# Kernel tuning notes

Hardware: AMD Instinct MI355X
Metric: run time of the kernel (lower is better)

## Reference

```python
import jax, jax.numpy as jnp
import numpy as np
from jax import lax

U = 64          # LSTM units (hard-coded in Actor)
EPS = 1e-12     # tf.contrib layer_norm default epsilon


def _ln(x, g, b):
    # layer norm over last axis; g,b broadcast
    mu = jnp.mean(x, axis=-1, keepdims=True)
    var = jnp.mean(jnp.square(x - mu), axis=-1, keepdims=True)
    return (x - mu) * jax.lax.rsqrt(var + EPS) * g + b


def _lstm_layer(xs, W, gamma, beta, gc, bc):
    # xs: (B, T, D); W: (D+U, 4U); gamma,beta: (4, U); gc,bc: (U,)
    B = xs.shape[0]
    c0 = jnp.zeros((B, U), xs.dtype)
    h0 = jnp.zeros((B, U), xs.dtype)

    def step(carry, x_t):
        c, h = carry
        z = jnp.concatenate([x_t, h], axis=-1) @ W          # (B, 4U), no bias
        z = _ln(z.reshape(B, 4, U), gamma, beta)            # per-gate layer norm
        i, j, f, o = z[:, 0], z[:, 1], z[:, 2], z[:, 3]
        new_c = c * jax.nn.sigmoid(f + 1.0) + jax.nn.sigmoid(i) * jnp.tanh(j)
        new_h = jnp.tanh(_ln(new_c, gc, bc)) * jax.nn.sigmoid(o)
        return (new_c, new_h), new_h

    _, hs = lax.scan(step, (c0, h0), jnp.swapaxes(xs, 0, 1))  # hs: (T, B, U)
    return jnp.swapaxes(hs, 0, 1)                             # (B, T, U)


def setup_inputs() -> dict:
    key = jax.random.key(0)
    ks = jax.random.split(key, 8)
    B, T, D, A = 256, 1024, 128, 16
    s1 = 1.0 / np.sqrt(D + U)
    s2 = 1.0 / np.sqrt(U + U)
    return {
        "obss": jax.random.normal(ks[0], (B, T, D), jnp.float32),
        "W1": jax.random.uniform(ks[1], (D + U, 4 * U), jnp.float32, -s1, s1),
        "gamma1": jnp.ones((4, U), jnp.float32),
        "beta1": jnp.zeros((4, U), jnp.float32),
        "gc1": jnp.ones((U,), jnp.float32),
        "bc1": jnp.zeros((U,), jnp.float32),
        "W2": jax.random.uniform(ks[2], (U + U, 4 * U), jnp.float32, -s2, s2),
        "gamma2": jnp.ones((4, U), jnp.float32),
        "beta2": jnp.zeros((4, U), jnp.float32),
        "gc2": jnp.ones((U,), jnp.float32),
        "bc2": jnp.zeros((U,), jnp.float32),
        "Wd": jax.random.uniform(ks[3], (U, A), jnp.float32, -0.003, 0.003),
        "bd": jnp.zeros((A,), jnp.float32),
    }


def reference(obss, W1, gamma1, beta1, gc1, bc1, W2, gamma2, beta2, gc2, bc2, Wd, bd):
    h1 = _lstm_layer(obss, W1, gamma1, beta1, gc1, bc1)   # (B, T, U)
    h2 = _lstm_layer(h1, W2, gamma2, beta2, gc2, bc2)     # (B, T, U)
    return jnp.tanh(h2 @ Wd + bd)                          # (B, T, nb_actions)
```

## Files before the change

### kernel.cpp

```cpp
#include <hip/hip_runtime.h>
#include <math.h>

#define TT 1024
#define DD 128
#define UU 64

__device__ __forceinline__ float sigm(float x) {
    return __builtin_amdgcn_rcpf(1.0f + __expf(-x));
}
__device__ __forceinline__ float tanhfast(float x) {
    float e = __expf(2.0f * x);
    return fmaf(-2.0f, __builtin_amdgcn_rcpf(e + 1.0f), 1.0f);
}

template<int CTRL>
__device__ __forceinline__ float dpp_add(float v) {
    return v + __int_as_float(__builtin_amdgcn_update_dpp(
        0, __float_as_int(v), CTRL, 0xf, 0xf, true));
}
__device__ __forceinline__ float wave_red_sum(float v) {
    v = dpp_add<0x111>(v);
    v = dpp_add<0x112>(v);
    v = dpp_add<0x114>(v);
    v = dpp_add<0x118>(v);
    v = dpp_add<0x142>(v);
    v = dpp_add<0x143>(v);
    return __int_as_float(__builtin_amdgcn_readlane(__float_as_int(v), 63));
}

#define DOT64(res, vptr, WARR) do {                                \
    const float4* _v4 = (const float4*)(vptr);                     \
    float _a0 = 0.f, _a1 = 0.f, _a2 = 0.f, _a3 = 0.f;              \
    _Pragma("unroll")                                              \
    for (int _k = 0; _k < UU / 4; ++_k) {                          \
        float4 _hv = _v4[_k];                                      \
        _a0 = fmaf(_hv.x, WARR[4 * _k + 0], _a0);                  \
        _a1 = fmaf(_hv.y, WARR[4 * _k + 1], _a1);                  \
        _a2 = fmaf(_hv.z, WARR[4 * _k + 2], _a2);                  \
        _a3 = fmaf(_hv.w, WARR[4 * _k + 3], _a3);                  \
    }                                                              \
    res = (_a0 + _a1) + (_a2 + _a3);                               \
} while (0)

__global__ __launch_bounds__(256, 1)
void xgemm(const float* __restrict__ obss, const float* __restrict__ W1,
           float* __restrict__ z1x, int t0, int chsh)
{
    const int tid = threadIdx.x;
    const int CH = 1 << chsh;
    __shared__ __align__(16) float xs[64 * DD];

    const int rbase = blockIdx.x * 64;
    for (int i = tid; i < 64 * (DD / 4); i += 256) {
        int rr = i >> 5;
        int k4 = i & 31;
        int r  = rbase + rr;
        int b  = r >> chsh;
        int tl = r & (CH - 1);
        ((float4*)xs)[rr * 32 + k4] =
            ((const float4*)(obss + ((size_t)b * TT + t0 + tl) * DD))[k4];
    }

    float w[DD];
    #pragma unroll
    for (int k = 0; k < DD; ++k) w[k] = W1[k * 256 + tid];
    __syncthreads();

    for (int rr = 0; rr < 64; rr += 2) {
        float a0=0,a1=0,a2=0,a3=0, b0=0,b1=0,b2=0,b3=0;
        const float4* x0 = (const float4*)(xs + rr * DD);
        const float4* x1 = (const float4*)(xs + (rr + 1) * DD);
        #pragma unroll
        for (int k4 = 0; k4 < DD / 4; ++k4) {
            float4 xv = x0[k4], yv = x1[k4];
            a0 = fmaf(xv.x, w[4*k4+0], a0);
            a1 = fmaf(xv.y, w[4*k4+1], a1);
            a2 = fmaf(xv.z, w[4*k4+2], a2);
            a3 = fmaf(xv.w, w[4*k4+3], a3);
            b0 = fmaf(yv.x, w[4*k4+0], b0);
            b1 = fmaf(yv.y, w[4*k4+1], b1);
            b2 = fmaf(yv.z, w[4*k4+2], b2);
            b3 = fmaf(yv.w, w[4*k4+3], b3);
        }
        size_t r = (size_t)rbase + rr;
        z1x[r * 256 + tid]       = (a0 + a1) + (a2 + a3);
        z1x[(r + 1) * 256 + tid] = (b0 + b1) + (b2 + b3);
    }
}

__global__ __launch_bounds__(768) __attribute__((amdgpu_waves_per_eu(3, 3)))
void lstm_rec(const float* __restrict__ z1x,
              const float* __restrict__ W1, const float* __restrict__ W2,
              const float* __restrict__ gamma1, const float* __restrict__ beta1,
              const float* __restrict__ gc1, const float* __restrict__ bc1,
              const float* __restrict__ gamma2, const float* __restrict__ beta2,
              const float* __restrict__ gc2, const float* __restrict__ bc2,
              const float* __restrict__ Wd, const float* __restrict__ bd,
              float* __restrict__ out, float* __restrict__ state,
              int t0, int nsteps)
{
    const int tid  = threadIdx.x;
    const int b    = blockIdx.x;
    const int gid  = tid >> 8;
    const int stid = tid & 255;
    const int lane = stid & 63;
    const int wav  = stid >> 6;

    __shared__ __align__(16) float zsA[256], zsB[256], z2xs[256];
    __shared__ __align__(16) float h1ring[2][UU];
    __shared__ __align__(16) float h1p[4][UU], h2p[4][UU];
    __shared__ __align__(16) float h2hist[32 * 65];
    __shared__ __align__(16) float wds[UU * 16];
    __shared__ float bds[16];

    float* st = state + (size_t)b * 256;
    const int NS = nsteps;

    if (gid == 0) {
        float w1h[UU];
        #pragma unroll
        for (int k = 0; k < UU; ++k) w1h[k] = W1[(DD + k) * 256 + stid];
        const float g1 = gamma1[stid], bb1 = beta1[stid];
        const float gcl = gc1[lane],  bcl = bc1[lane];

        float c1, h1v = 0.f;
        if (t0 == 0) { c1 = 0.f; h1p[wav][lane] = 0.f; }
        else         { c1 = st[lane]; h1v = st[64 + lane]; h1p[wav][lane] = h1v; }

        const float* zrow = z1x + (size_t)b * NS * 256;
        float zx = zrow[stid];
        __syncthreads();

        #pragma unroll 1
        for (int n = 0; n <= NS + 2; ++n) {
            float zxn = zx;
            if (n < NS) {
                int tnl = (n + 1 < NS) ? n + 1 : n;
                zxn = zrow[(size_t)tnl * 256 + stid];

                float zdot;
                DOT64(zdot, h1p[wav], w1h);
                float z = zx + zdot;
                float s = wave_red_sum(z);
                float q = wave_red_sum(z * z);
                float mu  = s * (1.f/64.f);
                float var = q * (1.f/64.f) - mu * mu;
                float zn  = (z - mu) * __builtin_amdgcn_rsqf(var + 1e-12f) * g1 + bb1;
                zsA[stid] = (wav == 1) ? tanhfast(zn)
                          : (wav == 2) ? sigm(zn + 1.f)
                          :              sigm(zn);
            }
            __syncthreads();
            if (n < NS) {
                float ai = zsA[lane],       aj = zsA[64 + lane];
                float af = zsA[128 + lane], ao = zsA[192 + lane];
                c1 = c1 * af + ai * aj;
                float cs = wave_red_sum(c1);
                float cq = wave_red_sum(c1 * c1);
                float cmu  = cs * (1.f/64.f);
                float cvar = cq * (1.f/64.f) - cmu * cmu;
                float cn   = (c1 - cmu) * __builtin_amdgcn_rsqf(cvar + 1e-12f) * gcl + bcl;
                h1v = tanhfast(cn) * ao;
                h1p[wav][lane] = h1v;
                if (wav == 0) h1ring[n & 1][lane] = h1v;
            }
            __syncthreads();
            zx = zxn;
        }
        if (t0 + NS < TT && wav == 0) {
            st[lane]      = c1;
            st[64 + lane] = h1v;
        }
    } else if (gid == 1) {
        float w2x[UU];
        #pragma unroll
        for (int k = 0; k < UU; ++k) w2x[k] = W2[k * 256 + stid];
        for (int i = stid; i < UU * 16; i += 256) wds[i] = Wd[i];
        if (stid < 16) bds[stid] = bd[stid];
        __syncthreads();

        #pragma unroll 1
        for (int n = 0; n <= NS + 2; ++n) {
            if (n >= 1 && n <= NS) {
                float zxdot;
                DOT64(zxdot, h1ring[(n - 1) & 1], w2x);
                z2xs[stid] = zxdot;
            }
            __syncthreads();
            if ((n & 15) == 2 && n >= 18) {
                int rloc = stid >> 4;
                int a    = stid & 15;
                int m    = n - 18 + rloc;
                float o = bds[a];
                const float* hrow = &h2hist[(m & 31) * 65];
                #pragma unroll
                for (int k = 0; k < UU; ++k)
                    o = fmaf(hrow[k], wds[k * 16 + a], o);
                out[((size_t)b * TT + (t0 + m)) * 16 + a] = tanhfast(o);
            }
            __syncthreads();
        }
    } else {
        float w2h[UU];
        #pragma unroll
        for (int k = 0; k < UU; ++k) w2h[k] = W2[(UU + k) * 256 + stid];
        const float g2 = gamma2[stid], bb2 = beta2[stid];
        const float gcl = gc2[lane],  bcl = bc2[lane];

        float c2, h2v = 0.f;
        if (t0 == 0) { c2 = 0.f; h2p[wav][lane] = 0.f; }
        else         { c2 = st[128 + lane]; h2v = st[192 + lane]; h2p[wav][lane] = h2v; }
        float z2h = 0.f;
        if (t0 != 0) { DOT64(z2h, h2p[wav], w2h); }
        __syncthreads();

        #pragma unroll 1
        for (int n = 0; n <= NS + 2; ++n) {
            if (n >= 2 && n <= NS + 1) {
                float ai = zsB[lane],       aj = zsB[64 + lane];
                float af = zsB[128 + lane], ao = zsB[192 + lane];
                c2 = c2 * af + ai * aj;
                float cs = wave_red_sum(c2);
                float cq = wave_red_sum(c2 * c2);
                float cmu  = cs * (1.f/64.f);
                float cvar = cq * (1.f/64.f) - cmu * cmu;
                float cn   = (c2 - cmu) * __builtin_amdgcn_rsqf(cvar + 1e-12f) * gcl + bcl;
                h2v = tanhfast(cn) * ao;
                h2p[wav][lane] = h2v;
                if (wav == 0) h2hist[((n - 2) & 31) * 65 + lane] = h2v;
                DOT64(z2h, h2p[wav], w2h);
            }
            __syncthreads();
            if (n >= 1 && n <= NS) {
                float z2 = z2xs[stid] + z2h;
                float s2 = wave_red_sum(z2);
                float q2 = wave_red_sum(z2 * z2);
                float mu2  = s2 * (1.f/64.f);
                float var2 = q2 * (1.f/64.f) - mu2 * mu2;
                float zn2  = (z2 - mu2) * __builtin_amdgcn_rsqf(var2 + 1e-12f) * g2 + bb2;
                zsB[stid] = (wav == 1) ? tanhfast(zn2)
                          : (wav == 2) ? sigm(zn2 + 1.f)
                          :              sigm(zn2);
            }
            __syncthreads();
        }
        if (t0 + NS < TT && wav == 0) {
            st[128 + lane] = c2;
            st[192 + lane] = h2v;
        }
    }
}

extern "C" void kernel_launch(void* const* d_in, const int* in_sizes, int n_in,
                              void* d_out, int out_size, void* d_ws, size_t ws_size,
                              hipStream_t stream) {
    (void)in_sizes; (void)n_in; (void)out_size;
    const float* obss   = (const float*)d_in[0];
    const float* W1     = (const float*)d_in[1];
    const float* gamma1 = (const float*)d_in[2];
    const float* beta1  = (const float*)d_in[3];
    const float* gc1    = (const float*)d_in[4];
    const float* bc1    = (const float*)d_in[5];
    const float* W2     = (const float*)d_in[6];
    const float* gamma2 = (const float*)d_in[7];
    const float* beta2  = (const float*)d_in[8];
    const float* gc2    = (const float*)d_in[9];
    const float* bc2    = (const float*)d_in[10];
    const float* Wd     = (const float*)d_in[11];
    const float* bd     = (const float*)d_in[12];
    float* out = (float*)d_out;

    float* state = (float*)d_ws;
    float* z1x   = (float*)((char*)d_ws + (size_t)256 * 256 * sizeof(float));

    int CH = 16;
    for (int c = TT; c >= 16; c >>= 1) {
        size_t need = (size_t)256 * c * 256 * sizeof(float)
                    + (size_t)256 * 256 * sizeof(float);
        if (need <= ws_size) { CH = c; break; }
    }
    int chsh = 31 - __builtin_clz((unsigned)CH);

    for (int t0 = 0; t0 < TT; t0 += CH) {
        xgemm<<<(256 * CH) / 64, 256, 0, stream>>>(obss, W1, z1x, t0, chsh);
        lstm_rec<<<256, 768, 0, stream>>>(z1x, W1, W2,
                                          gamma1, beta1, gc1, bc1,
                                          gamma2, beta2, gc2, bc2,
                                          Wd, bd, out, state, t0, CH);
    }
}
```

Before: 1.348 ms.

## Broadcast hidden state via readlane and move recurrent weights out of registers

The 64-float per-thread weight arrays are replaced. The recurrent weights for both layers now sit in shared memory as float4 and are read each step, and the layer-2 input weights are read straight from global memory (cached). The hidden state is no longer written to and reloaded from shared memory; each lane's value is broadcast with readlane inside the dot product. This cuts register pressure and an LDS round trip on the serial recurrence path, but adds LDS or global weight reads per step and 64 scalar readlane operations per dot product.

```diff
diff --git a/kernel.cpp b/kernel.cpp
--- a/kernel.cpp
+++ b/kernel.cpp
@@ -28,18 +28,31 @@
     return __int_as_float(__builtin_amdgcn_readlane(__float_as_int(v), 63));
 }
 
-#define DOT64(res, vptr, WARR) do {                                \
-    const float4* _v4 = (const float4*)(vptr);                     \
-    float _a0 = 0.f, _a1 = 0.f, _a2 = 0.f, _a3 = 0.f;              \
+#define RLF(H,K) __int_as_float(__builtin_amdgcn_readlane(__float_as_int(H), K))
+
+#define DOTLW(res, HV, WFP) do {                                   \
+    float a0 = 0.f, a1 = 0.f, a2 = 0.f, a3 = 0.f;                  \
     _Pragma("unroll")                                              \
-    for (int _k = 0; _k < UU / 4; ++_k) {                          \
-        float4 _hv = _v4[_k];                                      \
-        _a0 = fmaf(_hv.x, WARR[4 * _k + 0], _a0);                  \
-        _a1 = fmaf(_hv.y, WARR[4 * _k + 1], _a1);                  \
-        _a2 = fmaf(_hv.z, WARR[4 * _k + 2], _a2);                  \
-        _a3 = fmaf(_hv.w, WARR[4 * _k + 3], _a3);                  \
+    for (int _j = 0; _j < 16; ++_j) {                              \
+        float4 wq = (WFP)[_j * 256];                               \
+        a0 = fmaf(RLF(HV, 4*_j+0), wq.x, a0);                      \
+        a1 = fmaf(RLF(HV, 4*_j+1), wq.y, a1);                      \
+        a2 = fmaf(RLF(HV, 4*_j+2), wq.z, a2);                      \
+        a3 = fmaf(RLF(HV, 4*_j+3), wq.w, a3);                      \
     }                                                              \
-    res = (_a0 + _a1) + (_a2 + _a3);                               \
+    res = (a0 + a1) + (a2 + a3);                                   \
+} while (0)
+
+#define DOTGW(res, HV, GP) do {                                    \
+    float a0 = 0.f, a1 = 0.f, a2 = 0.f, a3 = 0.f;                  \
+    _Pragma("unroll")                                              \
+    for (int _j = 0; _j < 16; ++_j) {                              \
+        a0 = fmaf(RLF(HV, 4*_j+0), (GP)[(4*_j+0) * 256], a0);      \
+        a1 = fmaf(RLF(HV, 4*_j+1), (GP)[(4*_j+1) * 256], a1);      \
+        a2 = fmaf(RLF(HV, 4*_j+2), (GP)[(4*_j+2) * 256], a2);      \
+        a3 = fmaf(RLF(HV, 4*_j+3), (GP)[(4*_j+3) * 256], a3);      \
+    }                                                              \
+    res = (a0 + a1) + (a2 + a3);                                   \
 } while (0)
 
 __global__ __launch_bounds__(256, 1)
@@ -108,24 +121,32 @@
 
     __shared__ __align__(16) float zsA[256], zsB[256], z2xs[256];
     __shared__ __align__(16) float h1ring[2][UU];
-    __shared__ __align__(16) float h1p[4][UU], h2p[4][UU];
     __shared__ __align__(16) float h2hist[32 * 65];
     __shared__ __align__(16) float wds[UU * 16];
     __shared__ float bds[16];
+    __shared__ __align__(16) float4 wf4[2 * 16 * 256];
 
     float* st = state + (size_t)b * 256;
     const int NS = nsteps;
 
+    for (int i = tid; i < 2 * 16 * 256; i += 768) {
+        int m   = i >> 12;
+        int r   = i & 4095;
+        int j   = r >> 8;
+        int col = r & 255;
+        const float* src = (m == 0) ? &W1[(DD + 4 * j) * 256 + col]
+                                    : &W2[(UU + 4 * j) * 256 + col];
+        wf4[i] = make_float4(src[0], src[256], src[512], src[768]);
+    }
+
     if (gid == 0) {
-        float w1h[UU];
-        #pragma unroll
-        for (int k = 0; k < UU; ++k) w1h[k] = W1[(DD + k) * 256 + stid];
+        const float4* wfp = &wf4[stid];
         const float g1 = gamma1[stid], bb1 = beta1[stid];
         const float gcl = gc1[lane],  bcl = bc1[lane];
 
-        float c1, h1v = 0.f;
-        if (t0 == 0) { c1 = 0.f; h1p[wav][lane] = 0.f; }
-        else         { c1 = st[lane]; h1v = st[64 + lane]; h1p[wav][lane] = h1v; }
+        float c1, h1v;
+        if (t0 == 0) { c1 = 0.f; h1v = 0.f; }
+        else         { c1 = st[lane]; h1v = st[64 + lane]; }
 
         const float* zrow = z1x + (size_t)b * NS * 256;
         float zx = zrow[stid];
@@ -139,7 +160,7 @@
                 zxn = zrow[(size_t)tnl * 256 + stid];
 
                 float zdot;
-                DOT64(zdot, h1p[wav], w1h);
+                DOTLW(zdot, h1v, wfp);
                 float z = zx + zdot;
                 float s = wave_red_sum(z);
                 float q = wave_red_sum(z * z);
@@ -161,7 +182,6 @@
                 float cvar = cq * (1.f/64.f) - cmu * cmu;
                 float cn   = (c1 - cmu) * __builtin_amdgcn_rsqf(cvar + 1e-12f) * gcl + bcl;
                 h1v = tanhfast(cn) * ao;
-                h1p[wav][lane] = h1v;
                 if (wav == 0) h1ring[n & 1][lane] = h1v;
             }
             __syncthreads();
@@ -172,9 +192,7 @@
             st[64 + lane] = h1v;
         }
     } else if (gid == 1) {
-        float w2x[UU];
-        #pragma unroll
-        for (int k = 0; k < UU; ++k) w2x[k] = W2[k * 256 + stid];
+        const float* gp = W2 + stid;
         for (int i = stid; i < UU * 16; i += 256) wds[i] = Wd[i];
         if (stid < 16) bds[stid] = bd[stid];
         __syncthreads();
@@ -182,8 +200,9 @@
         #pragma unroll 1
         for (int n = 0; n <= NS + 2; ++n) {
             if (n >= 1 && n <= NS) {
+                float h1l = h1ring[(n - 1) & 1][lane];
                 float zxdot;
-                DOT64(zxdot, h1ring[(n - 1) & 1], w2x);
+                DOTGW(zxdot, h1l, gp);
                 z2xs[stid] = zxdot;
             }
             __syncthreads();
@@ -201,18 +220,16 @@
             __syncthreads();
         }
     } else {
-        float w2h[UU];
-        #pragma unroll
-        for (int k = 0; k < UU; ++k) w2h[k] = W2[(UU + k) * 256 + stid];
+        const float4* wfp = &wf4[4096 + stid];
         const float g2 = gamma2[stid], bb2 = beta2[stid];
         const float gcl = gc2[lane],  bcl = bc2[lane];
 
-        float c2, h2v = 0.f;
-        if (t0 == 0) { c2 = 0.f; h2p[wav][lane] = 0.f; }
-        else         { c2 = st[128 + lane]; h2v = st[192 + lane]; h2p[wav][lane] = h2v; }
+        float c2, h2v;
+        if (t0 == 0) { c2 = 0.f; h2v = 0.f; }
+        else         { c2 = st[128 + lane]; h2v = st[192 + lane]; }
+        __syncthreads();
         float z2h = 0.f;
-        if (t0 != 0) { DOT64(z2h, h2p[wav], w2h); }
-        __syncthreads();
+        if (t0 != 0) { DOTLW(z2h, h2v, wfp); }
 
         #pragma unroll 1
         for (int n = 0; n <= NS + 2; ++n) {
@@ -226,9 +243,8 @@
                 float cvar = cq * (1.f/64.f) - cmu * cmu;
                 float cn   = (c2 - cmu) * __builtin_amdgcn_rsqf(cvar + 1e-12f) * gcl + bcl;
                 h2v = tanhfast(cn) * ao;
-                h2p[wav][lane] = h2v;
                 if (wav == 0) h2hist[((n - 2) & 31) * 65 + lane] = h2v;
-                DOT64(z2h, h2p[wav], w2h);
+                DOTLW(z2h, h2v, wfp);
             }
             __syncthreads();
             if (n >= 1 && n <= NS) {
```

Result: slower. 1.721 ms (+27.6%).

## Merge warp-specialized LSTM groups into single 256-thread sequential per-step loop

Applied to the files above, without the earlier changes.

Replaces the 768-thread block with three specialized 256-thread groups (layer-1 recurrence, layer-2 input projection plus output dense, layer-2 recurrence) with one 256-thread group that runs both layers in sequence each timestep. Each thread now holds all three weight columns in registers, and the cross-group pipelining skew and h1 ring buffer are removed. The aim is to cut barrier cost over many waves and the pipeline bookkeeping. The trade-off is a longer serial critical path per step and higher register pressure.

```diff
diff --git a/kernel.cpp b/kernel.cpp
--- a/kernel.cpp
+++ b/kernel.cpp
@@ -88,7 +88,7 @@
     }
 }
 
-__global__ __launch_bounds__(768) __attribute__((amdgpu_waves_per_eu(3, 3)))
+__global__ __launch_bounds__(256, 1)
 void lstm_rec(const float* __restrict__ z1x,
               const float* __restrict__ W1, const float* __restrict__ W2,
               const float* __restrict__ gamma1, const float* __restrict__ beta1,
@@ -101,13 +101,10 @@
 {
     const int tid  = threadIdx.x;
     const int b    = blockIdx.x;
-    const int gid  = tid >> 8;
-    const int stid = tid & 255;
-    const int lane = stid & 63;
-    const int wav  = stid >> 6;
-
-    __shared__ __align__(16) float zsA[256], zsB[256], z2xs[256];
-    __shared__ __align__(16) float h1ring[2][UU];
+    const int lane = tid & 63;
+    const int wav  = tid >> 6;
+
+    __shared__ __align__(16) float zsA[256], zsB[256];
     __shared__ __align__(16) float h1p[4][UU], h2p[4][UU];
     __shared__ __align__(16) float h2hist[32 * 65];
     __shared__ __align__(16) float wds[UU * 16];
@@ -116,138 +113,128 @@
     float* st = state + (size_t)b * 256;
     const int NS = nsteps;
 
-    if (gid == 0) {
-        float w1h[UU];
+    float w1h[UU], w2x[UU], w2h[UU];
+    #pragma unroll
+    for (int k = 0; k < UU; ++k) w1h[k] = W1[(DD + k) * 256 + tid];
+    #pragma unroll
+    for (int k = 0; k < UU; ++k) w2x[k] = W2[k * 256 + tid];
+    #pragma unroll
+    for (int k = 0; k < UU; ++k) w2h[k] = W2[(UU + k) * 256 + tid];
+
+    const float g1 = gamma1[tid],  bb1 = beta1[tid];
+    const float g2 = gamma2[tid],  bb2 = beta2[tid];
+    const float gcl1 = gc1[lane],  bcl1 = bc1[lane];
+    const float gcl2 = gc2[lane],  bcl2 = bc2[lane];
+
+    for (int i = tid; i < UU * 16; i += 256) wds[i] = Wd[i];
+    if (tid < 16) bds[tid] = bd[tid];
+
+    float c1, c2, h1v, h2v;
+    if (t0 == 0) { c1 = 0.f; c2 = 0.f; h1v = 0.f; h2v = 0.f; }
+    else {
+        c1 = st[lane];        h1v = st[64 + lane];
+        c2 = st[128 + lane];  h2v = st[192 + lane];
+    }
+    h1p[wav][lane] = h1v;
+    h2p[wav][lane] = h2v;
+    float z2h = 0.f;
+    if (t0 != 0) { DOT64(z2h, h2p[wav], w2h); }
+
+    const float* zrow = z1x + (size_t)b * NS * 256;
+    float zx = zrow[tid];
+    __syncthreads();
+
+    #pragma unroll 1
+    for (int n = 0; n < NS; ++n) {
+        float zxn = (n + 1 < NS) ? zrow[(size_t)(n + 1) * 256 + tid] : zx;
+
+        float zdot;
+        DOT64(zdot, h1p[wav], w1h);
+        float z = zx + zdot;
+        float s = wave_red_sum(z);
+        float q = wave_red_sum(z * z);
+        float mu  = s * (1.f/64.f);
+        float var = q * (1.f/64.f) - mu * mu;
+        float zn  = (z - mu) * __builtin_amdgcn_rsqf(var + 1e-12f) * g1 + bb1;
+        zsA[tid] = (wav == 1) ? tanhfast(zn)
+                 : (wav == 2) ? sigm(zn + 1.f)
+                 :              sigm(zn);
+
+        if ((n & 15) == 2 && n >= 18) {
+            int rloc = tid >> 4;
+            int a    = tid & 15;
+            int m    = n - 18 + rloc;
+            float o = bds[a];
+            const float* hrow = &h2hist[(m & 31) * 65];
+            #pragma unroll
+            for (int k = 0; k < UU; ++k)
+                o = fmaf(hrow[k], wds[k * 16 + a], o);
+            out[((size_t)b * TT + (t0 + m)) * 16 + a] = tanhfast(o);
+        }
+        __syncthreads();
+
+        {
+            float ai = zsA[lane],       aj = zsA[64 + lane];
+            float af = zsA[128 + lane], ao = zsA[192 + lane];
+            c1 = c1 * af + ai * aj;
+            float cs = wave_red_sum(c1);
+            float cq = wave_red_sum(c1 * c1);
+            float cmu  = cs * (1.f/64.f);
+            float cvar = cq * (1.f/64.f) - cmu * cmu;
+            float cn   = (c1 - cmu) * __builtin_amdgcn_rsqf(cvar + 1e-12f) * gcl1 + bcl1;
+            h1v = tanhfast(cn) * ao;
+            h1p[wav][lane] = h1v;
+        }
+        {
+            float z2x;
+            DOT64(z2x, h1p[wav], w2x);
+            float z2 = z2x + z2h;
+            float s2 = wave_red_sum(z2);
+            float q2 = wave_red_sum(z2 * z2);
+            float mu2  = s2 * (1.f/64.f);
+            float var2 = q2 * (1.f/64.f) - mu2 * mu2;
+            float zn2  = (z2 - mu2) * __builtin_amdgcn_rsqf(var2 + 1e-12f) * g2 + bb2;
+            zsB[tid] = (wav == 1) ? tanhfast(zn2)
+                     : (wav == 2) ? sigm(zn2 + 1.f)
+                     :              sigm(zn2);
+        }
+        __syncthreads();
+
+        {
+            float ai = zsB[lane],       aj = zsB[64 + lane];
+            float af = zsB[128 + lane], ao = zsB[192 + lane];
+            c2 = c2 * af + ai * aj;
+            float cs = wave_red_sum(c2);
+            float cq = wave_red_sum(c2 * c2);
+            float cmu  = cs * (1.f/64.f);
+            float cvar = cq * (1.f/64.f) - cmu * cmu;
+            float cn   = (c2 - cmu) * __builtin_amdgcn_rsqf(cvar + 1e-12f) * gcl2 + bcl2;
+            h2v = tanhfast(cn) * ao;
+            h2p[wav][lane] = h2v;
+            if (wav == 0) h2hist[(n & 31) * 65 + lane] = h2v;
+            DOT64(z2h, h2p[wav], w2h);
+        }
+        zx = zxn;
+    }
+
+    __syncthreads();
+    {
+        int rloc = tid >> 4;
+        int a    = tid & 15;
+        int m    = NS - 16 + rloc;
+        float o = bds[a];
+        const float* hrow = &h2hist[(m & 31) * 65];
         #pragma unroll
-        for (int k = 0; k < UU; ++k) w1h[k] = W1[(DD + k) * 256 + stid];
-        const float g1 = gamma1[stid], bb1 = beta1[stid];
-        const float gcl = gc1[lane],  bcl = bc1[lane];
-
-        float c1, h1v = 0.f;
-        if (t0 == 0) { c1 = 0.f; h1p[wav][lane] = 0.f; }
-        else         { c1 = st[lane]; h1v = st[64 + lane]; h1p[wav][lane] = h1v; }
-
-        const float* zrow = z1x + (size_t)b * NS * 256;
-        float zx = zrow[stid];
-        __syncthreads();
-
-        #pragma unroll 1
-        for (int n = 0; n <= NS + 2; ++n) {
-            float zxn = zx;
-            if (n < NS) {
-                int tnl = (n + 1 < NS) ? n + 1 : n;
-                zxn = zrow[(size_t)tnl * 256 + stid];
-
-                float zdot;
-                DOT64(zdot, h1p[wav], w1h);
-                float z = zx + zdot;
-                float s = wave_red_sum(z);
-                float q = wave_red_sum(z * z);
-                float mu  = s * (1.f/64.f);
-                float var = q * (1.f/64.f) - mu * mu;
-                float zn  = (z - mu) * __builtin_amdgcn_rsqf(var + 1e-12f) * g1 + bb1;
-                zsA[stid] = (wav == 1) ? tanhfast(zn)
-                          : (wav == 2) ? sigm(zn + 1.f)
-                          :              sigm(zn);
-            }
-            __syncthreads();
-            if (n < NS) {
-                float ai = zsA[lane],       aj = zsA[64 + lane];
-                float af = zsA[128 + lane], ao = zsA[192 + lane];
-                c1 = c1 * af + ai * aj;
-                float cs = wave_red_sum(c1);
-                float cq = wave_red_sum(c1 * c1);
-                float cmu  = cs * (1.f/64.f);
-                float cvar = cq * (1.f/64.f) - cmu * cmu;
-                float cn   = (c1 - cmu) * __builtin_amdgcn_rsqf(cvar + 1e-12f) * gcl + bcl;
-                h1v = tanhfast(cn) * ao;
-                h1p[wav][lane] = h1v;
-                if (wav == 0) h1ring[n & 1][lane] = h1v;
-            }
-            __syncthreads();
-            zx = zxn;
-        }
-        if (t0 + NS < TT && wav == 0) {
-            st[lane]      = c1;
-            st[64 + lane] = h1v;
-        }
-    } else if (gid == 1) {
-        float w2x[UU];
-        #pragma unroll
-        for (int k = 0; k < UU; ++k) w2x[k] = W2[k * 256 + stid];
-        for (int i = stid; i < UU * 16; i += 256) wds[i] = Wd[i];
-        if (stid < 16) bds[stid] = bd[stid];
-        __syncthreads();
-
-        #pragma unroll 1
-        for (int n = 0; n <= NS + 2; ++n) {
-            if (n >= 1 && n <= NS) {
-                float zxdot;
-                DOT64(zxdot, h1ring[(n - 1) & 1], w2x);
-                z2xs[stid] = zxdot;
-            }
-            __syncthreads();
-            if ((n & 15) == 2 && n >= 18) {
-                int rloc = stid >> 4;
-                int a    = stid & 15;
-                int m    = n - 18 + rloc;
-                float o = bds[a];
-                const float* hrow = &h2hist[(m & 31) * 65];
-                #pragma unroll
-                for (int k = 0; k < UU; ++k)
-                    o = fmaf(hrow[k], wds[k * 16 + a], o);
-                out[((size_t)b * TT + (t0 + m)) * 16 + a] = tanhfast(o);
-            }
-            __syncthreads();
-        }
-    } else {
-        float w2h[UU];
-        #pragma unroll
-        for (int k = 0; k < UU; ++k) w2h[k] = W2[(UU + k) * 256 + stid];
-        const float g2 = gamma2[stid], bb2 = beta2[stid];
-        const float gcl = gc2[lane],  bcl = bc2[lane];
-
-        float c2, h2v = 0.f;
-        if (t0 == 0) { c2 = 0.f; h2p[wav][lane] = 0.f; }
-        else         { c2 = st[128 + lane]; h2v = st[192 + lane]; h2p[wav][lane] = h2v; }
-        float z2h = 0.f;
-        if (t0 != 0) { DOT64(z2h, h2p[wav], w2h); }
-        __syncthreads();
-
-        #pragma unroll 1
-        for (int n = 0; n <= NS + 2; ++n) {
-            if (n >= 2 && n <= NS + 1) {
-                float ai = zsB[lane],       aj = zsB[64 + lane];
-                float af = zsB[128 + lane], ao = zsB[192 + lane];
-                c2 = c2 * af + ai * aj;
-                float cs = wave_red_sum(c2);
-                float cq = wave_red_sum(c2 * c2);
-                float cmu  = cs * (1.f/64.f);
-                float cvar = cq * (1.f/64.f) - cmu * cmu;
-                float cn   = (c2 - cmu) * __builtin_amdgcn_rsqf(cvar + 1e-12f) * gcl + bcl;
-                h2v = tanhfast(cn) * ao;
-                h2p[wav][lane] = h2v;
-                if (wav == 0) h2hist[((n - 2) & 31) * 65 + lane] = h2v;
-                DOT64(z2h, h2p[wav], w2h);
-            }
-            __syncthreads();
-            if (n >= 1 && n <= NS) {
-                float z2 = z2xs[stid] + z2h;
-                float s2 = wave_red_sum(z2);
-                float q2 = wave_red_sum(z2 * z2);
-                float mu2  = s2 * (1.f/64.f);
-                float var2 = q2 * (1.f/64.f) - mu2 * mu2;
-                float zn2  = (z2 - mu2) * __builtin_amdgcn_rsqf(var2 + 1e-12f) * g2 + bb2;
-                zsB[stid] = (wav == 1) ? tanhfast(zn2)
-                          : (wav == 2) ? sigm(zn2 + 1.f)
-                          :              sigm(zn2);
-            }
-            __syncthreads();
-        }
-        if (t0 + NS < TT && wav == 0) {
-            st[128 + lane] = c2;
-            st[192 + lane] = h2v;
-        }
+        for (int k = 0; k < UU; ++k)
+            o = fmaf(hrow[k], wds[k * 16 + a], o);
+        out[((size_t)b * TT + (t0 + m)) * 16 + a] = tanhfast(o);
+    }
+
+    if (t0 + NS < TT && wav == 0) {
+        st[lane]       = c1;
+        st[64 + lane]  = h1v;
+        st[128 + lane] = c2;
+        st[192 + lane] = h2v;
     }
 }
 
@@ -283,7 +270,7 @@
 
     for (int t0 = 0; t0 < TT; t0 += CH) {
         xgemm<<<(256 * CH) / 64, 256, 0, stream>>>(obss, W1, z1x, t0, chsh);
-        lstm_rec<<<256, 768, 0, stream>>>(z1x, W1, W2,
+        lstm_rec<<<256, 256, 0, stream>>>(z1x, W1, W2,
                                           gamma1, beta1, gc1, bc1,
                                           gamma2, beta2, gc2, bc2,
                                           Wd, bd, out, state, t0, CH);
```

Measured after the change: 1.993 ms. 1.48x slower.
